# Kernel optimization log

Hardware: AMD Instinct MI355X
Metric: run time of the kernel (lower is better)

The kernel has to match this reference:

```python
import jax, jax.numpy as jnp
import numpy as np

D_MODEL = 1024
N_HEAD = 16
D_QKV = 64
INIT_RANGE = 0.02
BOUND = float(np.sqrt(3.0) * INIT_RANGE)
SCALE = 1.0 / D_QKV ** 0.5


def setup_inputs() -> dict:
    key = jax.random.key(0)
    kx, k1, k2, k3, k4 = jax.random.split(key, 5)
    B, T = 4, 2048
    x = jax.random.normal(kx, (B, T, D_MODEL), dtype=jnp.float32)
    half_f = D_MODEL // 2
    half_a = D_QKV // 2
    u = lambda k, shp: jax.random.uniform(k, shp, dtype=jnp.float32, minval=-BOUND, maxval=BOUND)
    w_qkv_c = u(k1, (N_HEAD, half_f, 3, half_a))
    w_qkv_p = u(k2, (N_HEAD, half_f, 3, half_a))
    w_o_c = u(k3, (N_HEAD, half_a, half_f))
    w_o_p = u(k4, (N_HEAD, half_a, half_f))
    return {"x": x, "w_qkv_c": w_qkv_c, "w_qkv_p": w_qkv_p, "w_o_c": w_o_c, "w_o_p": w_o_p}


def reference(x, w_qkv_c, w_qkv_p, w_o_c, w_o_p):
    x_c, x_p = jnp.split(x, 2, axis=-1)  # [B,T,d_model//2] each
    # partitioned QKV projections: [B,H,T,3,a/2]
    qkv_c = jnp.einsum('btf,hfca->bhtca', x_c, w_qkv_c)
    qkv_p = jnp.einsum('btf,hfca->bhtca', x_p, w_qkv_p)
    q_c, k_c, v_c = qkv_c[:, :, :, 0], qkv_c[:, :, :, 1], qkv_c[:, :, :, 2]
    q_p, k_p, v_p = qkv_p[:, :, :, 0], qkv_p[:, :, :, 1], qkv_p[:, :, :, 2]
    q = jnp.concatenate([q_c, q_p], axis=-1) * SCALE  # [B,H,T,d_qkv]
    k = jnp.concatenate([k_c, k_p], axis=-1)
    v = jnp.concatenate([v_c, v_p], axis=-1)
    dots = jnp.einsum('bhqa,bhka->bhqk', q, k)  # [B,H,T,T]
    probs = jax.nn.softmax(dots, axis=-1)
    o = jnp.einsum('bhqk,bhka->bhqa', probs, v)  # [B,H,T,d_qkv]
    o_c, o_p = jnp.split(o, 2, axis=-1)
    out_c = jnp.einsum('bhta,haf->btf', o_c, w_o_c)
    out_p = jnp.einsum('bhta,haf->btf', o_p, w_o_p)
    return (out_c, out_p)
```

## Files before the change

### kernel.cpp

```cpp
#include <hip/hip_runtime.h>


typedef __attribute__((ext_vector_type(8))) short bf16x8;
typedef __attribute__((ext_vector_type(4))) float f32x4;
typedef unsigned short u16;

#define QSCALE 0.18033688011112042f

__device__ __forceinline__ u16 f2bf(float f){
  unsigned u = __builtin_bit_cast(unsigned, f);
  u += 0x7FFFu + ((u >> 16) & 1u);
  return (u16)(u >> 16);
}

__device__ __forceinline__ unsigned cvtpk(float lo, float hi){
  unsigned r;
  asm("v_cvt_pk_bf16_f32 %0, %1, %2" : "=v"(r) : "v"(lo), "v"(hi));
  return r;
}

__device__ __forceinline__ void gload16(const void* g, void* l){
  __builtin_amdgcn_global_load_lds(
    (const __attribute__((address_space(1))) unsigned*)g,
    (__attribute__((address_space(3))) unsigned*)l, 16, 0, 0);
}

__global__ __launch_bounds__(256) void k_prep(const float4* __restrict__ x, u16* __restrict__ xA,
                                              const float* __restrict__ wqc, const float* __restrict__ wqp,
                                              u16* __restrict__ wqt,
                                              const float* __restrict__ woc, const float* __restrict__ wop,
                                              u16* __restrict__ wot){
  const unsigned blk = blockIdx.x;
  if (blk < 8192u){
    unsigned i = blk*256 + threadIdx.x;
    float4 v = x[i];
    unsigned j = i*4;
    unsigned row = j >> 10, col = j & 1023u;
    unsigned tile = row >> 4, li = row & 15u;
    unsigned part = col >> 9, ks = (col >> 5) & 15u, lg = (col >> 3) & 3u, e = col & 7u;
    uint2 pk;
    pk.x = (unsigned)f2bf(v.x) | ((unsigned)f2bf(v.y) << 16);
    pk.y = (unsigned)f2bf(v.z) | ((unsigned)f2bf(v.w) << 16);
    *(uint2*)(xA + (size_t)(((tile*2 + part)*16 + ks)*512) + li*32 + lg*8 + e) = pk;
  } else if (blk < 14336u){
    unsigned i = (blk - 8192u)*256 + threadIdx.x;
    unsigned ph = i / 49152u;
    unsigned r  = i - ph*49152u;
    unsigned ks = r / 3072u;
    unsigned r2 = r - ks*3072u;
    unsigned n  = r2 >> 9;
    unsigned r3 = r2 & 511u;
    unsigned lg = r3 >> 7, li = (r3 >> 3) & 15u, e = r3 & 7u;
    unsigned h = ph & 15u;
    unsigned f = ks*32u + lg*8u + e;
    const float* src = (ph < 16) ? wqc : wqp;
    wqt[i] = f2bf(src[h*49152u + f*96u + (n>>1)*32u + (n&1u)*16u + li]);
  } else {
    unsigned i = (blk - 14336u)*256 + threadIdx.x;
    unsigned e = i & 7u;
    unsigned lane = (i >> 3) & 63u;
    unsigned n  = (i >> 9) & 7u;
    unsigned ks = (i >> 12) & 15u;
    unsigned ft = (i >> 16) & 3u;
    unsigned part = i >> 18;
    unsigned f = ft*128u + n*16u + (lane & 15u);
    unsigned a = (lane >> 4)*8u + e;
    const float* src = part ? wop : woc;
    wot[i] = f2bf(src[ks*16384u + a*512u + f]);
  }
}

__global__ __launch_bounds__(256) void k_qkv(const u16* __restrict__ xA, const u16* __restrict__ wt,
                                             u16* __restrict__ Q, u16* __restrict__ K, u16* __restrict__ VT){
  const int lane = threadIdx.x & 63, wv = threadIdx.x >> 6;
  const int lg = lane >> 4, li = lane & 15;
  const int blk = blockIdx.x;
  const int xcd = blk & 7, idx = blk >> 3;
  const int tt  = (idx >> 5)*8 + xcd;
  const int ph  = idx & 31;
  const int row0 = tt*256 + wv*64;
  const int part = ph >> 4, h = ph & 15;

  f32x4 acc[4][6] = {};
  const u16* wbase = wt + (size_t)ph*49152;
  const unsigned aoff = (unsigned)(li*32 + lg*8);
  #pragma unroll 2
  for (int ks = 0; ks < 16; ++ks){
    bf16x8 a[4], b[6];
    #pragma unroll
    for (int m=0;m<4;++m)
      a[m] = *(const bf16x8*)(xA + (size_t)(((tt*16 + wv*4 + m)*2 + part)*16 + ks)*512 + aoff);
    #pragma unroll
    for (int n=0;n<6;++n)
      b[n] = *(const bf16x8*)(wbase + ks*3072 + n*512 + lane*8);
    #pragma unroll
    for (int m=0;m<4;++m)
      #pragma unroll
      for (int n=0;n<6;++n)
        acc[m][n] = __builtin_amdgcn_mfma_f32_16x16x32_bf16(a[m], b[n], acc[m][n], 0, 0, 0);
  }

  const int b_ = row0 >> 11;
  const int bh = b_*16 + h;
  const int tl0 = (row0 & 2047) + lg*4;
  #pragma unroll
  for (int m=0;m<4;++m){
    #pragma unroll
    for (int n=0;n<6;++n){
      const int c = n >> 1;
      const int af = part*32 + (n & 1)*16 + li;
      if (c == 2){
        uint2 pk;
        pk.x = (unsigned)f2bf(acc[m][n][0]) | ((unsigned)f2bf(acc[m][n][1]) << 16);
        pk.y = (unsigned)f2bf(acc[m][n][2]) | ((unsigned)f2bf(acc[m][n][3]) << 16);
        const int c2 = (m&1)*2 + (lg>>1);
        char* dst = (char*)VT + (size_t)bh*262144
                  + (size_t)(((row0 & 2047) >> 5) + (m>>1))*4096
                  + af*64 + ((c2 ^ (af&3))<<4) + (lg&1)*8;
        *(uint2*)dst = pk;
      } else {
        u16* dst = (c == 0) ? Q : K;
        const float sc = (c == 0) ? QSCALE : 1.0f;
        #pragma unroll
        for (int r=0;r<4;++r){
          int tl = tl0 + m*16 + r;
          dst[((size_t)bh*2048 + tl)*64 + af] = f2bf(acc[m][n][r] * sc);
        }
      }
    }
  }
}

#define NKT 64
#define PLD 40
__global__ __launch_bounds__(256, 4) void k_attn(const u16* __restrict__ Q, const u16* __restrict__ K,
                                                 const u16* __restrict__ VT, u16* __restrict__ OA){
  __shared__ __align__(16) char smem[36864];
  const int lane = threadIdx.x & 63, w = threadIdx.x >> 6;
  const int lg = lane >> 4, li = lane & 15;
  const int swz = (blockIdx.x & 7)*128 + (blockIdx.x >> 3);
  const int bh = swz >> 4, qt = swz & 15;
  const int q0 = qt*128 + w*32;

  const char* Kg = (const char*)(K + (size_t)bh*131072);
  const char* Vg = (const char*)VT + (size_t)bh*262144;
  const u16*  Qb = Q + (size_t)bh*131072;
  u16* pw = (u16*)(smem + 16384) + w*2560;

  const unsigned ksrc = (unsigned)((w*8 + (lane>>3))*128 + (((lane&7) ^ (lane>>3)) << 4));
  const unsigned vsrc = (unsigned)(w*1024 + lane*16);
  const unsigned ldst = (unsigned)(w*1024);

  const unsigned kc0 = (unsigned)(((     lg) ^ (li&7)) << 4);
  const unsigned kc1 = (unsigned)(((4 +  lg) ^ (li&7)) << 4);
  const unsigned vc  = (unsigned)(((lg) ^ (li&3)) << 4);

  bf16x8 aq[2][2];
  #pragma unroll
  for (int m=0;m<2;++m)
    #pragma unroll
    for (int kd=0;kd<2;++kd)
      aq[m][kd] = *(const bf16x8*)(Qb + (size_t)(q0 + m*16 + li)*64 + kd*32 + lg*8);

  const short one_bf = (short)0x3F80;
  bf16x8 ones = {one_bf,one_bf,one_bf,one_bf,one_bf,one_bf,one_bf,one_bf};

  f32x4 o[2][4] = {};
  f32x4 ls[2] = {};

  auto QKEXP = [&](const char* sK, u16* pW){
    #pragma unroll
    for (int n=0;n<2;++n){
      bf16x8 bk0 = *(const bf16x8*)(sK + (n*16 + li)*128 + kc0);
      bf16x8 bk1 = *(const bf16x8*)(sK + (n*16 + li)*128 + kc1);
      #pragma unroll
      for (int m=0;m<2;++m){
        f32x4 s = {0.f,0.f,0.f,0.f};
        s = __builtin_amdgcn_mfma_f32_16x16x32_bf16(bk0, aq[m][0], s, 0, 0, 0);
        s = __builtin_amdgcn_mfma_f32_16x16x32_bf16(bk1, aq[m][1], s, 0, 0, 0);
        uint2 pk;
        pk.x = cvtpk(__builtin_exp2f(s[0]), __builtin_exp2f(s[1]));
        pk.y = cvtpk(__builtin_exp2f(s[2]), __builtin_exp2f(s[3]));
        *(uint2*)(pW + (size_t)(m*16 + li)*PLD + n*16 + lg*4) = pk;
      }
    }
  };
  auto PV = [&](const char* sV, const u16* pR){
    bf16x8 pa0 = *(const bf16x8*)(pR + (size_t)(     li)*PLD + lg*8);
    bf16x8 pa1 = *(const bf16x8*)(pR + (size_t)(16 + li)*PLD + lg*8);
    __builtin_amdgcn_s_setprio(1);
    #pragma unroll
    for (int nd=0;nd<4;++nd){
      bf16x8 bv = *(const bf16x8*)(sV + (nd*16 + li)*64 + vc);
      o[0][nd] = __builtin_amdgcn_mfma_f32_16x16x32_bf16(pa0, bv, o[0][nd], 0, 0, 0);
      o[1][nd] = __builtin_amdgcn_mfma_f32_16x16x32_bf16(pa1, bv, o[1][nd], 0, 0, 0);
    }
    ls[0] = __builtin_amdgcn_mfma_f32_16x16x32_bf16(pa0, ones, ls[0], 0, 0, 0);
    ls[1] = __builtin_amdgcn_mfma_f32_16x16x32_bf16(pa1, ones, ls[1], 0, 0, 0);
    __builtin_amdgcn_s_setprio(0);
  };

  gload16(Kg + ksrc,          smem + ldst);
  gload16(Vg + vsrc,          smem + 8192 + ldst);
  gload16(Kg + 4096u + ksrc,  smem + 4096 + ldst);
  asm volatile("s_waitcnt vmcnt(0)" ::: "memory");
  __builtin_amdgcn_s_barrier();
  QKEXP(smem, pw);
  __builtin_amdgcn_s_barrier();

  for (int kt = 0; kt < NKT-1; ++kt){
    const int pr = kt & 1, pn = pr ^ 1;
    gload16(Vg + (kt+1)*4096u + vsrc, smem + 8192 + pn*4096 + ldst);
    if (kt + 2 < NKT)
      gload16(Kg + (kt+2)*4096u + ksrc, smem + pr*4096 + ldst);
    QKEXP(smem + pn*4096, pw + pn*1280);
    PV(smem + 8192 + pr*4096, pw + pr*1280);
    asm volatile("s_waitcnt vmcnt(0)" ::: "memory");
    __builtin_amdgcn_s_barrier();
  }
  PV(smem + 8192 + ((NKT-1)&1)*4096, pw + ((NKT-1)&1)*1280);

  const int b_ = bh >> 4, h = bh & 15;
  #pragma unroll
  for (int m=0;m<2;++m){
    const int tile = (b_*2048 + q0 + m*16) >> 4;
    #pragma unroll
    for (int r=0;r<4;++r){
      float linv = 1.0f / ls[m][r];
      #pragma unroll
      for (int nd=0;nd<4;++nd){
        OA[(size_t)(((tile*16 + h)*2 + (nd>>1))*512)
           + (lg*4 + r)*32 + ((nd&1)*2 + (li>>3))*8 + (li&7)] = f2bf(o[m][nd][r] * linv);
      }
    }
  }
}

__global__ __launch_bounds__(256) void k_proj(const u16* __restrict__ OA, const u16* __restrict__ wot,
                                              float* __restrict__ out){
  const int lane = threadIdx.x & 63, wv = threadIdx.x >> 6;
  const int lg = lane >> 4, li = lane & 15;
  const int blk = blockIdx.x;
  const int xcd = blk & 7, idx = blk >> 3;
  const int rowTile = (idx >> 3)*8 + xcd;
  const int colTile = idx & 7;
  const int row0 = rowTile*128 + wv*32;
  const int part = colTile >> 2;
  const int ft   = colTile & 3;
  const int f0   = ft*128;

  f32x4 acc[2][8] = {};
  const u16* wbase = wot + (size_t)part*262144 + (size_t)ft*65536;
  const unsigned aoff = (unsigned)(li*32 + lg*8);
  #pragma unroll 4
  for (int ks = 0; ks < 16; ++ks){
    bf16x8 a[2];
    #pragma unroll
    for (int m=0;m<2;++m)
      a[m] = *(const bf16x8*)(OA + (size_t)((((rowTile*8 + wv*2 + m)*16 + ks)*2 + part)*512) + aoff);
    #pragma unroll
    for (int n=0;n<8;++n){
      bf16x8 b = *(const bf16x8*)(wbase + ks*4096 + n*512 + lane*8);
      #pragma unroll
      for (int m=0;m<2;++m)
        acc[m][n] = __builtin_amdgcn_mfma_f32_16x16x32_bf16(a[m], b, acc[m][n], 0, 0, 0);
    }
  }
  float* obp = out + (size_t)part*(8192u*512u);
  #pragma unroll
  for (int m=0;m<2;++m)
    #pragma unroll
    for (int n=0;n<8;++n)
      #pragma unroll
      for (int r=0;r<4;++r)
        obp[(size_t)(row0 + m*16 + lg*4 + r)*512 + f0 + n*16 + li] = acc[m][n][r];
}

extern "C" void kernel_launch(void* const* d_in, const int* in_sizes, int n_in,
                              void* d_out, int out_size, void* d_ws, size_t ws_size,
                              hipStream_t stream){
  const float* x   = (const float*)d_in[0];
  const float* wqc = (const float*)d_in[1];
  const float* wqp = (const float*)d_in[2];
  const float* woc = (const float*)d_in[3];
  const float* wop = (const float*)d_in[4];

  char* ws = (char*)d_ws;
  u16* xA  = (u16*)(ws);
  u16* Q   = (u16*)(ws + 16777216);
  u16* K   = (u16*)(ws + 2*16777216);
  u16* VT  = (u16*)(ws + 3*16777216);
  u16* wqt = (u16*)(ws + 4*16777216);
  u16* wot = (u16*)(ws + 4*16777216 + 3145728);
  u16* OA  = xA;
  float* out = (float*)d_out;

  k_prep <<<16384, 256, 0, stream>>>((const float4*)x, xA, wqc, wqp, wqt, woc, wop, wot);
  k_qkv  <<<1024,  256, 0, stream>>>(xA, wqt, Q, K, VT);
  k_attn <<<1024,  256, 0, stream>>>(Q, K, VT, OA);
  k_proj <<<512,   256, 0, stream>>>(OA, wot, out);
}
```

Measured before the change: 174.2 us.

## Pre-swizzle K into MFMA fragment layout and load it directly into registers

The QKV projection now writes K in a fragment-ordered layout, so each lane of the attention kernel can fetch its MFMA B operands with coalesced 16-byte global loads straight into registers. This drops the LDS staging buffer for K and the LDS reads of K fragments, shrinking shared memory from 36 KB to 28 KB. The loop is unrolled by two so the register double-buffer of K fragments can be indexed statically. In exchange, every wave loads the full K tile into its own registers, which costs more global and L2 traffic and more VGPRs, and the load latency is now exposed to register dependencies instead of going through the async LDS path.

```diff
diff --git a/kernel.cpp b/kernel.cpp
--- a/kernel.cpp
+++ b/kernel.cpp
@@ -118,13 +118,18 @@
                   + (size_t)(((row0 & 2047) >> 5) + (m>>1))*4096
                   + af*64 + ((c2 ^ (af&3))<<4) + (lg&1)*8;
         *(uint2*)dst = pk;
-      } else {
-        u16* dst = (c == 0) ? Q : K;
-        const float sc = (c == 0) ? QSCALE : 1.0f;
+      } else if (c == 1){
+        const unsigned kb = ((unsigned)(af>>5))*512 + ((unsigned)((af>>3)&3))*128 + (unsigned)(af&7);
         #pragma unroll
         for (int r=0;r<4;++r){
-          int tl = tl0 + m*16 + r;
-          dst[((size_t)bh*2048 + tl)*64 + af] = f2bf(acc[m][n][r] * sc);
+          int t = tl0 + m*16 + r;
+          K[(size_t)bh*131072 + (t>>5)*2048 + ((t>>4)&1)*1024 + kb + (t&15)*8] = f2bf(acc[m][n][r]);
+        }
+      } else {
+        #pragma unroll
+        for (int r=0;r<4;++r){
+          int t = tl0 + m*16 + r;
+          Q[((size_t)bh*2048 + t)*64 + af] = f2bf(acc[m][n][r] * QSCALE);
         }
       }
     }
@@ -135,25 +140,21 @@
 #define PLD 40
 __global__ __launch_bounds__(256, 4) void k_attn(const u16* __restrict__ Q, const u16* __restrict__ K,
                                                  const u16* __restrict__ VT, u16* __restrict__ OA){
-  __shared__ __align__(16) char smem[36864];
+  __shared__ __align__(16) char smem[28672];
   const int lane = threadIdx.x & 63, w = threadIdx.x >> 6;
   const int lg = lane >> 4, li = lane & 15;
   const int swz = (blockIdx.x & 7)*128 + (blockIdx.x >> 3);
   const int bh = swz >> 4, qt = swz & 15;
   const int q0 = qt*128 + w*32;
 
-  const char* Kg = (const char*)(K + (size_t)bh*131072);
-  const char* Vg = (const char*)VT + (size_t)bh*262144;
-  const u16*  Qb = Q + (size_t)bh*131072;
-  u16* pw = (u16*)(smem + 16384) + w*2560;
-
-  const unsigned ksrc = (unsigned)((w*8 + (lane>>3))*128 + (((lane&7) ^ (lane>>3)) << 4));
+  const char* Kfb = (const char*)K + (size_t)bh*262144;
+  const char* Vg  = (const char*)VT + (size_t)bh*262144;
+  const u16*  Qb  = Q + (size_t)bh*131072;
+  u16* pw = (u16*)(smem + 8192) + w*2560;
+
   const unsigned vsrc = (unsigned)(w*1024 + lane*16);
   const unsigned ldst = (unsigned)(w*1024);
-
-  const unsigned kc0 = (unsigned)(((     lg) ^ (li&7)) << 4);
-  const unsigned kc1 = (unsigned)(((4 +  lg) ^ (li&7)) << 4);
-  const unsigned vc  = (unsigned)(((lg) ^ (li&3)) << 4);
+  const unsigned vc   = (unsigned)(((lg) ^ (li&3)) << 4);
 
   bf16x8 aq[2][2];
   #pragma unroll
@@ -167,12 +168,20 @@
 
   f32x4 o[2][4] = {};
   f32x4 ls[2] = {};
-
-  auto QKEXP = [&](const char* sK, u16* pW){
+  bf16x8 ka0_00, ka0_01, ka0_10, ka0_11;
+  bf16x8 ka1_00, ka1_01, ka1_10, ka1_11;
+
+#define KLOAD(BANK, KT) { const char* kb_ = Kfb + (size_t)(KT)*4096; \
+    ka##BANK##_00 = *(const bf16x8*)(kb_ +        lane*16); \
+    ka##BANK##_01 = *(const bf16x8*)(kb_ + 1024 + lane*16); \
+    ka##BANK##_10 = *(const bf16x8*)(kb_ + 2048 + lane*16); \
+    ka##BANK##_11 = *(const bf16x8*)(kb_ + 3072 + lane*16); }
+
+  auto QKEXP = [&](bf16x8 b00, bf16x8 b01, bf16x8 b10, bf16x8 b11, u16* pW){
     #pragma unroll
     for (int n=0;n<2;++n){
-      bf16x8 bk0 = *(const bf16x8*)(sK + (n*16 + li)*128 + kc0);
-      bf16x8 bk1 = *(const bf16x8*)(sK + (n*16 + li)*128 + kc1);
+      bf16x8 bk0 = n ? b10 : b00;
+      bf16x8 bk1 = n ? b11 : b01;
       #pragma unroll
       for (int m=0;m<2;++m){
         f32x4 s = {0.f,0.f,0.f,0.f};
@@ -200,25 +209,28 @@
     __builtin_amdgcn_s_setprio(0);
   };
 
-  gload16(Kg + ksrc,          smem + ldst);
-  gload16(Vg + vsrc,          smem + 8192 + ldst);
-  gload16(Kg + 4096u + ksrc,  smem + 4096 + ldst);
+#define AITER(KT, PR, PN) { \
+    gload16(Vg + (size_t)((KT)+1)*4096u + vsrc, smem + (PN)*4096 + ldst); \
+    if ((KT) + 2 < NKT) KLOAD(PR, (KT)+2); \
+    QKEXP(ka##PN##_00, ka##PN##_01, ka##PN##_10, ka##PN##_11, pw + (PN)*1280); \
+    PV(smem + (PR)*4096, pw + (PR)*1280); \
+    asm volatile("s_waitcnt vmcnt(0)" ::: "memory"); \
+    __builtin_amdgcn_s_barrier(); }
+
+  gload16(Vg + vsrc, smem + ldst);
+  KLOAD(0, 0);
+  KLOAD(1, 1);
   asm volatile("s_waitcnt vmcnt(0)" ::: "memory");
   __builtin_amdgcn_s_barrier();
-  QKEXP(smem, pw);
+  QKEXP(ka0_00, ka0_01, ka0_10, ka0_11, pw);
   __builtin_amdgcn_s_barrier();
 
-  for (int kt = 0; kt < NKT-1; ++kt){
-    const int pr = kt & 1, pn = pr ^ 1;
-    gload16(Vg + (kt+1)*4096u + vsrc, smem + 8192 + pn*4096 + ldst);
-    if (kt + 2 < NKT)
-      gload16(Kg + (kt+2)*4096u + ksrc, smem + pr*4096 + ldst);
-    QKEXP(smem + pn*4096, pw + pn*1280);
-    PV(smem + 8192 + pr*4096, pw + pr*1280);
-    asm volatile("s_waitcnt vmcnt(0)" ::: "memory");
-    __builtin_amdgcn_s_barrier();
-  }
-  PV(smem + 8192 + ((NKT-1)&1)*4096, pw + ((NKT-1)&1)*1280);
+  for (int base = 0; base < NKT-2; base += 2){
+    AITER(base,   0, 1);
+    AITER(base+1, 1, 0);
+  }
+  AITER(NKT-2, 0, 1);
+  PV(smem + 4096, pw + 1280);
 
   const int b_ = bh >> 4, h = bh & 15;
   #pragma unroll
@@ -234,6 +246,8 @@
       }
     }
   }
+#undef AITER
+#undef KLOAD
 }
 
 __global__ __launch_bounds__(256) void k_proj(const u16* __restrict__ OA, const u16* __restrict__ wot,
```

Measured after the change: 171.3 us. No clear change (-1.7%).
